# Performance work log

Measured on AMD Instinct MI355X. Metric: run time of the kernel, lower is better.

Reference implementation:

```python
import jax, jax.numpy as jnp
import numpy as np

B, N, E = 16, 5000, 160000
IN, OUT, H = 64, 64, 1  # heads=1 (GATConv default)
NEG_SLOPE = 0.2


def setup_inputs() -> dict:
    key = jax.random.key(0)
    ks = jax.random.split(key, 10)
    data = jax.random.normal(ks[0], (B, N, IN), jnp.float32)
    # random edges with no self-loops (PyG removes then re-adds self-loops;
    # with no pre-existing self-loops this matches exactly)
    src = jax.random.randint(ks[1], (E,), 0, N)
    off = jax.random.randint(ks[2], (E,), 1, N)
    dst = (src + off) % N
    edge_index = jnp.stack([src, dst]).astype(jnp.int32)
    edge_attr = jax.random.uniform(ks[3], (E,), jnp.float32)
    # GATConv parameters (glorot-ish init)
    W = jax.random.normal(ks[4], (H * OUT, IN), jnp.float32) / np.sqrt(IN)
    W_edge = jax.random.normal(ks[5], (H * OUT, 1), jnp.float32)
    att_src = jax.random.normal(ks[6], (1, H, OUT), jnp.float32) * 0.1
    att_dst = jax.random.normal(ks[7], (1, H, OUT), jnp.float32) * 0.1
    att_edge = jax.random.normal(ks[8], (1, H, OUT), jnp.float32) * 0.1
    bias = jnp.zeros((H * OUT,), jnp.float32)
    return {"data": data, "edge_index": edge_index, "edge_attr": edge_attr,
            "W": W, "W_edge": W_edge, "att_src": att_src, "att_dst": att_dst,
            "att_edge": att_edge, "bias": bias}


def reference(data, edge_index, edge_attr, W, W_edge, att_src, att_dst, att_edge, bias):
    BN = B * N
    x = data.reshape(BN, IN)
    # faithful to source: tile edges per batch WITHOUT node offset
    ei = jnp.tile(edge_index, (1, B))          # [2, B*E]
    ea = jnp.tile(edge_attr, B)[:, None]        # [B*E, 1]
    # add self-loops for all BN nodes, edge_attr filled with mean
    loops = jnp.arange(BN, dtype=ei.dtype)
    src = jnp.concatenate([ei[0], loops])       # [Etot]
    dst = jnp.concatenate([ei[1], loops])
    ea = jnp.concatenate([ea, jnp.full((BN, 1), ea.mean(), ea.dtype)])
    # linear transforms
    xl = (x @ W.T).reshape(BN, H, OUT)          # [BN, H, C]
    a_src = (xl * att_src).sum(-1)              # [BN, H]
    a_dst = (xl * att_dst).sum(-1)
    e_emb = (ea @ W_edge.T).reshape(-1, H, OUT) # [Etot, H, C]
    a_edge = (e_emb * att_edge).sum(-1)         # [Etot, H]
    # per-edge attention + segment softmax over destination nodes
    alpha = a_src[src] + a_dst[dst] + a_edge
    alpha = jax.nn.leaky_relu(alpha, NEG_SLOPE)
    amax = jax.ops.segment_max(alpha, dst, num_segments=BN)
    alpha = jnp.exp(alpha - amax[dst])
    denom = jax.ops.segment_sum(alpha, dst, num_segments=BN)
    alpha = alpha / (denom[dst] + 1e-16)
    # message passing: gather src features, weight, scatter-sum to dst
    msg = xl[src] * alpha[:, :, None]           # [Etot, H, C]
    out = jax.ops.segment_sum(msg, dst, num_segments=BN)
    out = out.reshape(BN, H * OUT) + bias
    return out.reshape(B, N, OUT), jnp.stack([src, dst]), alpha
```

## Files before the change

### kernel.cpp

```cpp
#include <hip/hip_runtime.h>

#define NN 5000
#define EE 160000
#define BNN 80000
#define BEE 2560000
#define ETOT 2640000
#define CAP 128
#define POISON ((int)0xAAAAAAAA)

#define K1_FILL 625
#define K1_GEMM 79
#define K1_SUM  80
#define K1_BLKS (K1_FILL + K1_GEMM + K1_SUM)

#define K2_GATHER 1250
#define K2_GEMMHI 1172
#define K2_OUT1   2578
#define K2_BLKS   (K2_GATHER + K2_GEMMHI + K2_OUT1)

#define K3_BLKS 1290

typedef __attribute__((ext_vector_type(8))) short short8;
typedef __attribute__((ext_vector_type(4))) float floatx4;

__device__ __forceinline__ short8 pack_bf8(const float* p) {
    union { unsigned int u[4]; short8 s; } r;
    #pragma unroll
    for (int j = 0; j < 4; ++j) {
        unsigned int lo = __float_as_uint(p[2 * j]) >> 16;
        unsigned int hi = __float_as_uint(p[2 * j + 1]) & 0xFFFF0000u;
        r.u[j] = lo | hi;
    }
    return r.s;
}

template <bool LO>
__device__ __forceinline__ void gemm_tile(
        int gblk, int t,
        const float* __restrict__ x, const float* __restrict__ W,
        const float* __restrict__ att_src, const float* __restrict__ att_dst,
        const float* __restrict__ bias,
        float* __restrict__ xl, float* __restrict__ asrc, float* __restrict__ adst,
        float* __restrict__ out0) {
    const int wave = t >> 6;
    const int lane = t & 63;
    const int quad = lane >> 4;
    const int col  = lane & 15;
    short8 bfrag[4][2];
    float attsv[4], attdv[4], biasv[4];
    #pragma unroll
    for (int ct = 0; ct < 4; ++ct) {
        int c = ct * 16 + col;
        #pragma unroll
        for (int ks = 0; ks < 2; ++ks)
            bfrag[ct][ks] = pack_bf8(W + c * 64 + ks * 32 + quad * 8);
        if (LO) { attsv[ct] = att_src[c]; attdv[ct] = att_dst[c]; }
        else    { biasv[ct] = bias[c]; }
    }
    int node0 = (gblk * 4 + wave) << 4;
    short8 afrag[2];
    const float* xrow = x + (size_t)(node0 + col) * 64;
    #pragma unroll
    for (int ks = 0; ks < 2; ++ks)
        afrag[ks] = pack_bf8(xrow + ks * 32 + quad * 8);
    floatx4 acc[4];
    #pragma unroll
    for (int ct = 0; ct < 4; ++ct) acc[ct] = (floatx4){0.f, 0.f, 0.f, 0.f};
    #pragma unroll
    for (int ks = 0; ks < 2; ++ks)
        #pragma unroll
        for (int ct = 0; ct < 4; ++ct)
            acc[ct] = __builtin_amdgcn_mfma_f32_16x16x32_bf16(afrag[ks], bfrag[ct][ks], acc[ct], 0, 0, 0);
    if (LO) {
        float ps[4] = {0.f,0.f,0.f,0.f}, pd[4] = {0.f,0.f,0.f,0.f};
        #pragma unroll
        for (int r = 0; r < 4; ++r) {
            int node = node0 + quad * 4 + r;
            #pragma unroll
            for (int ct = 0; ct < 4; ++ct) {
                float v = acc[ct][r];
                if (node < NN) xl[node * 64 + ct * 16 + col] = v;
                ps[r] += v * attsv[ct];
                pd[r] += v * attdv[ct];
            }
        }
        #pragma unroll
        for (int off = 1; off < 16; off <<= 1) {
            #pragma unroll
            for (int r = 0; r < 4; ++r) {
                ps[r] += __shfl_xor(ps[r], off, 64);
                pd[r] += __shfl_xor(pd[r], off, 64);
            }
        }
        if (col == 0) {
            #pragma unroll
            for (int r = 0; r < 4; ++r) {
                int node = node0 + quad * 4 + r;
                if (node < NN) { asrc[node] = ps[r]; adst[node] = pd[r]; }
            }
        }
    } else {
        #pragma unroll
        for (int r = 0; r < 4; ++r) {
            int node = node0 + quad * 4 + r;
            #pragma unroll
            for (int ct = 0; ct < 4; ++ct) {
                float v = acc[ct][r];
                if (node >= NN) out0[node * 64 + ct * 16 + col] = v + biasv[ct];
            }
        }
    }
}

__global__ __launch_bounds__(256) void k1(
        const float* __restrict__ x, const float* __restrict__ W,
        const float* __restrict__ att_src, const float* __restrict__ att_dst,
        const float* __restrict__ ea, const float* __restrict__ wedge,
        const float* __restrict__ atte, const int* __restrict__ ei,
        float* __restrict__ xl, float* __restrict__ asrc, float* __restrict__ adst,
        int* __restrict__ cursor, int* __restrict__ bucket, float* __restrict__ eabuf,
        float* __restrict__ partials) {
    __shared__ float red[256];
    const int blk = blockIdx.x;
    const int t = threadIdx.x;
    if (blk < K1_FILL) {
        int e = blk * 256 + t;
        int s = ei[e];
        int d = ei[EE + e];
        float ev = ea[e];
        int pos = atomicAdd(&cursor[d], 1) - POISON;
        if (pos < CAP) {
            bucket[d * CAP + pos] = (s << 18) | e;
            eabuf[d * CAP + pos] = ev;
        }
    } else if (blk < K1_FILL + K1_GEMM) {
        gemm_tile<true>(blk - K1_FILL, t, x, W, att_src, att_dst, nullptr,
                        xl, asrc, adst, nullptr);
    } else {
        int sb = blk - (K1_FILL + K1_GEMM);
        int gid = sb * 256 + t;
        float v = 0.f;
        for (int i = gid; i < EE; i += K1_SUM * 256) v += ea[i];
        red[t] = v;
        __syncthreads();
        #pragma unroll
        for (int off = 128; off > 0; off >>= 1) {
            if (t < off) red[t] += red[t + off];
            __syncthreads();
        }
        if (t == 0) partials[sb] = red[0];
        if (sb == 0 && t < 64) {
            float s = wedge[t] * atte[t];
            #pragma unroll
            for (int off = 32; off > 0; off >>= 1) s += __shfl_xor(s, off, 64);
            if (t == 0) partials[80] = s;
        }
    }
}

__global__ __launch_bounds__(256) void k2(
        const float* __restrict__ x, const float* __restrict__ W,
        const float* __restrict__ bias,
        const int* __restrict__ ei,
        const int* __restrict__ bucket, const float* __restrict__ eabuf,
        const int* __restrict__ cursor,
        const float* __restrict__ asrc, const float* __restrict__ adst,
        const float* __restrict__ partials,
        const float* __restrict__ xl,
        float* __restrict__ albuf, float* __restrict__ selfal,
        float* __restrict__ out0, float* __restrict__ out1) {
    __shared__ float s_r[4][CAP];
    __shared__ int   s_se[4][CAP];
    __shared__ int   s_e[4][CAP];
    const int blk = blockIdx.x;
    const int t = threadIdx.x, w = t >> 6, lane = t & 63;

    if (blk < K2_GATHER) {
        float s0 = 0.f;
        #pragma unroll
        for (int i = 0; i < 80; ++i) s0 += partials[i];
        float s1 = partials[80];
        float selfadd = s0 * (1.0f / EE) * s1;
        float bl = bias[lane];
        int d = blk * 4 + w;
        float* sr = s_r[w]; int* sse = s_se[w]; int* se_ = s_e[w];
        int deg = min(cursor[d] - POISON, CAP);
        float ad = adst[d];
        float rs = asrc[d] + ad + selfadd;
        rs = (rs > 0.f) ? rs : 0.2f * rs;
        float rmax = rs;
        for (int base = 0; base < deg; base += 64) {
            int idx = base + lane;
            if (idx < deg) {
                int packed = bucket[d * CAP + idx];
                float ev   = eabuf[d * CAP + idx];
                int se = packed >> 18;
                int e  = packed & 0x3FFFF;
                float r = asrc[se] + ad + ev * s1;
                r = (r > 0.f) ? r : 0.2f * r;
                sr[idx] = r; sse[idx] = se; se_[idx] = e;
                rmax = fmaxf(rmax, r);
            }
        }
        #pragma unroll
        for (int off = 32; off > 0; off >>= 1) rmax = fmaxf(rmax, __shfl_xor(rmax, off, 64));
        float m = rmax;
        float es = __expf(rs - m);
        float l = es;
        float acc = es * xl[d * 64 + lane];
        int j = 0;
        for (; j + 4 <= deg; j += 4) {
            int a0 = sse[j], a1 = sse[j + 1], a2 = sse[j + 2], a3 = sse[j + 3];
            float x0 = xl[a0 * 64 + lane], x1 = xl[a1 * 64 + lane];
            float x2 = xl[a2 * 64 + lane], x3 = xl[a3 * 64 + lane];
            float w0 = __expf(sr[j] - m),     w1 = __expf(sr[j + 1] - m);
            float w2 = __expf(sr[j + 2] - m), w3 = __expf(sr[j + 3] - m);
            acc += 16.0f * (w0 * x0 + w1 * x1 + w2 * x2 + w3 * x3);
            l   += 16.0f * (w0 + w1 + w2 + w3);
        }
        for (; j < deg; ++j) {
            float w0 = __expf(sr[j] - m);
            acc += 16.0f * w0 * xl[sse[j] * 64 + lane];
            l   += 16.0f * w0;
        }
        float inv = 1.0f / (l + 1e-16f);
        out0[d * 64 + lane] = acc * inv + bl;
        if (lane == 0) selfal[d] = es * inv;
        for (int idx = lane; idx < deg; idx += 64)
            albuf[se_[idx]] = __expf(sr[idx] - m) * inv;
    } else if (blk < K2_GATHER + K2_GEMMHI) {
        gemm_tile<false>(78 + (blk - K2_GATHER), t, x, W, nullptr, nullptr, bias,
                         nullptr, nullptr, nullptr, out0);
    } else {
        int qb = blk - (K2_GATHER + K2_GEMMHI);
        for (int q = qb * 256 + t; q < ETOT / 4; q += K2_OUT1 * 256) {
            int i = q * 4;
            float4 sv, dv;
            if (i < BEE) {
                int oe = i % EE;
                int4 s4 = *reinterpret_cast<const int4*>(ei + oe);
                int4 d4 = *reinterpret_cast<const int4*>(ei + EE + oe);
                sv = make_float4((float)s4.x, (float)s4.y, (float)s4.z, (float)s4.w);
                dv = make_float4((float)d4.x, (float)d4.y, (float)d4.z, (float)d4.w);
            } else {
                int nn = i - BEE;
                sv = make_float4((float)nn, (float)(nn+1), (float)(nn+2), (float)(nn+3));
                dv = sv;
            }
            *reinterpret_cast<float4*>(out1 + i) = sv;
            *reinterpret_cast<float4*>(out1 + ETOT + i) = dv;
        }
    }
}

__global__ __launch_bounds__(256) void k3(
        const float* __restrict__ albuf, const float* __restrict__ selfal,
        float* __restrict__ out2) {
    for (int q = blockIdx.x * 256 + threadIdx.x; q < ETOT / 4; q += K3_BLKS * 256) {
        int i = q * 4;
        float4 av;
        if (i < BEE) {
            av = *reinterpret_cast<const float4*>(albuf + (i % EE));
        } else {
            float a[4];
            #pragma unroll
            for (int jj = 0; jj < 4; ++jj) {
                int nn = i + jj - BEE;
                a[jj] = (nn < NN) ? selfal[nn] : 1.0f;
            }
            av = make_float4(a[0], a[1], a[2], a[3]);
        }
        *reinterpret_cast<float4*>(out2 + i) = av;
    }
}

extern "C" void kernel_launch(void* const* d_in, const int* in_sizes, int n_in,
                              void* d_out, int out_size, void* d_ws, size_t ws_size,
                              hipStream_t stream) {
    const float* data  = (const float*)d_in[0];
    const int*   ei    = (const int*)d_in[1];
    const float* ea    = (const float*)d_in[2];
    const float* W     = (const float*)d_in[3];
    const float* atts  = (const float*)d_in[5];
    const float* attd  = (const float*)d_in[6];
    const float* atte  = (const float*)d_in[7];
    const float* bias  = (const float*)d_in[8];
    const float* wedge = (const float*)d_in[4];

    float* out0 = (float*)d_out;
    float* out1 = out0 + 5120000;
    float* out2 = out0 + 10400000;

    float* ws = (float*)d_ws;
    float* xl       = ws;
    float* asrc     = ws + 320000;
    float* adst     = ws + 325000;
    float* albuf    = ws + 330000;
    float* selfal   = ws + 490000;
    float* partials = ws + 495000;
    int*   cursor   = (int*)(ws + 495082);
    int*   bucket   = (int*)(ws + 500082);
    float* eabuf    = ws + 1140082;

    k1<<<K1_BLKS, 256, 0, stream>>>(data, W, atts, attd, ea, wedge, atte, ei,
                                    xl, asrc, adst, cursor, bucket, eabuf, partials);
    k2<<<K2_BLKS, 256, 0, stream>>>(data, W, bias, ei, bucket, eabuf, cursor,
                                    asrc, adst, partials, xl,
                                    albuf, selfal, out0, out1);
    k3<<<K3_BLKS, 256, 0, stream>>>(albuf, selfal, out2);
}
```

Baseline: 130.1 us.

## Drop third kernel by scattering alpha directly and move high GEMM into k1

Removes the k3 launch and the albuf/selfal staging buffers. The gather kernel now writes each edge's alpha straight into all 16 batch replicas of out2, and the constant-one self-loop alphas are filled by the out1 blocks. The high-node GEMM tiles move from k2 to k1 so they overlap with bucket filling, and large output writes use nontemporal stores. In exchange, the 16-way alpha writes are scattered strided stores rather than coalesced float4 copies, which may cost write efficiency.

```diff
diff --git a/kernel.cpp b/kernel.cpp
--- a/kernel.cpp
+++ b/kernel.cpp
@@ -8,17 +8,15 @@
 #define CAP 128
 #define POISON ((int)0xAAAAAAAA)
 
-#define K1_FILL 625
-#define K1_GEMM 79
-#define K1_SUM  80
-#define K1_BLKS (K1_FILL + K1_GEMM + K1_SUM)
+#define K1_FILL   625
+#define K1_GEMMLO 79
+#define K1_SUM    80
+#define K1_GEMMHI 1172
+#define K1_BLKS (K1_FILL + K1_GEMMLO + K1_SUM + K1_GEMMHI)
 
 #define K2_GATHER 1250
-#define K2_GEMMHI 1172
 #define K2_OUT1   2578
-#define K2_BLKS   (K2_GATHER + K2_GEMMHI + K2_OUT1)
-
-#define K3_BLKS 1290
+#define K2_BLKS   (K2_GATHER + K2_OUT1)
 
 typedef __attribute__((ext_vector_type(8))) short short8;
 typedef __attribute__((ext_vector_type(4))) float floatx4;
@@ -32,6 +30,11 @@
         r.u[j] = lo | hi;
     }
     return r.s;
+}
+
+__device__ __forceinline__ void nt_store4(float a, float b, float c, float d, float* p) {
+    floatx4 v = {a, b, c, d};
+    __builtin_nontemporal_store(v, reinterpret_cast<floatx4*>(p));
 }
 
 template <bool LO>
@@ -106,7 +109,9 @@
             #pragma unroll
             for (int ct = 0; ct < 4; ++ct) {
                 float v = acc[ct][r];
-                if (node >= NN) out0[node * 64 + ct * 16 + col] = v + biasv[ct];
+                if (node >= NN)
+                    __builtin_nontemporal_store(v + biasv[ct],
+                                                &out0[node * 64 + ct * 16 + col]);
             }
         }
     }
@@ -115,9 +120,11 @@
 __global__ __launch_bounds__(256) void k1(
         const float* __restrict__ x, const float* __restrict__ W,
         const float* __restrict__ att_src, const float* __restrict__ att_dst,
+        const float* __restrict__ bias,
         const float* __restrict__ ea, const float* __restrict__ wedge,
         const float* __restrict__ atte, const int* __restrict__ ei,
         float* __restrict__ xl, float* __restrict__ asrc, float* __restrict__ adst,
+        float* __restrict__ out0,
         int* __restrict__ cursor, int* __restrict__ bucket, float* __restrict__ eabuf,
         float* __restrict__ partials) {
     __shared__ float red[256];
@@ -133,11 +140,11 @@
             bucket[d * CAP + pos] = (s << 18) | e;
             eabuf[d * CAP + pos] = ev;
         }
-    } else if (blk < K1_FILL + K1_GEMM) {
+    } else if (blk < K1_FILL + K1_GEMMLO) {
         gemm_tile<true>(blk - K1_FILL, t, x, W, att_src, att_dst, nullptr,
                         xl, asrc, adst, nullptr);
-    } else {
-        int sb = blk - (K1_FILL + K1_GEMM);
+    } else if (blk < K1_FILL + K1_GEMMLO + K1_SUM) {
+        int sb = blk - (K1_FILL + K1_GEMMLO);
         int gid = sb * 256 + t;
         float v = 0.f;
         for (int i = gid; i < EE; i += K1_SUM * 256) v += ea[i];
@@ -155,11 +162,14 @@
             for (int off = 32; off > 0; off >>= 1) s += __shfl_xor(s, off, 64);
             if (t == 0) partials[80] = s;
         }
+    } else {
+        int gblk = 78 + (blk - (K1_FILL + K1_GEMMLO + K1_SUM));
+        gemm_tile<false>(gblk, t, x, W, nullptr, nullptr, bias,
+                         nullptr, nullptr, nullptr, out0);
     }
 }
 
 __global__ __launch_bounds__(256) void k2(
-        const float* __restrict__ x, const float* __restrict__ W,
         const float* __restrict__ bias,
         const int* __restrict__ ei,
         const int* __restrict__ bucket, const float* __restrict__ eabuf,
@@ -167,8 +177,8 @@
         const float* __restrict__ asrc, const float* __restrict__ adst,
         const float* __restrict__ partials,
         const float* __restrict__ xl,
-        float* __restrict__ albuf, float* __restrict__ selfal,
-        float* __restrict__ out0, float* __restrict__ out1) {
+        float* __restrict__ out0, float* __restrict__ out1,
+        float* __restrict__ out2) {
     __shared__ float s_r[4][CAP];
     __shared__ int   s_se[4][CAP];
     __shared__ int   s_e[4][CAP];
@@ -224,53 +234,35 @@
             l   += 16.0f * w0;
         }
         float inv = 1.0f / (l + 1e-16f);
-        out0[d * 64 + lane] = acc * inv + bl;
-        if (lane == 0) selfal[d] = es * inv;
-        for (int idx = lane; idx < deg; idx += 64)
-            albuf[se_[idx]] = __expf(sr[idx] - m) * inv;
-    } else if (blk < K2_GATHER + K2_GEMMHI) {
-        gemm_tile<false>(78 + (blk - K2_GATHER), t, x, W, nullptr, nullptr, bias,
-                         nullptr, nullptr, nullptr, out0);
+        __builtin_nontemporal_store(acc * inv + bl, &out0[d * 64 + lane]);
+        if (lane == 0) out2[BEE + d] = es * inv;
+        for (int idx = lane; idx < deg; idx += 64) {
+            float a = __expf(sr[idx] - m) * inv;
+            float* p = out2 + se_[idx];
+            #pragma unroll
+            for (int b = 0; b < 16; ++b) p[b * EE] = a;
+        }
     } else {
-        int qb = blk - (K2_GATHER + K2_GEMMHI);
+        int qb = blk - K2_GATHER;
+        {
+            int idx = qb * 256 + t;
+            if (idx < (BNN - NN) / 4)
+                nt_store4(1.f, 1.f, 1.f, 1.f, out2 + BEE + NN + idx * 4);
+        }
         for (int q = qb * 256 + t; q < ETOT / 4; q += K2_OUT1 * 256) {
             int i = q * 4;
-            float4 sv, dv;
             if (i < BEE) {
                 int oe = i % EE;
                 int4 s4 = *reinterpret_cast<const int4*>(ei + oe);
                 int4 d4 = *reinterpret_cast<const int4*>(ei + EE + oe);
-                sv = make_float4((float)s4.x, (float)s4.y, (float)s4.z, (float)s4.w);
-                dv = make_float4((float)d4.x, (float)d4.y, (float)d4.z, (float)d4.w);
+                nt_store4((float)s4.x, (float)s4.y, (float)s4.z, (float)s4.w, out1 + i);
+                nt_store4((float)d4.x, (float)d4.y, (float)d4.z, (float)d4.w, out1 + ETOT + i);
             } else {
                 int nn = i - BEE;
-                sv = make_float4((float)nn, (float)(nn+1), (float)(nn+2), (float)(nn+3));
-                dv = sv;
-            }
-            *reinterpret_cast<float4*>(out1 + i) = sv;
-            *reinterpret_cast<float4*>(out1 + ETOT + i) = dv;
-        }
-    }
-}
-
-__global__ __launch_bounds__(256) void k3(
-        const float* __restrict__ albuf, const float* __restrict__ selfal,
-        float* __restrict__ out2) {
-    for (int q = blockIdx.x * 256 + threadIdx.x; q < ETOT / 4; q += K3_BLKS * 256) {
-        int i = q * 4;
-        float4 av;
-        if (i < BEE) {
-            av = *reinterpret_cast<const float4*>(albuf + (i % EE));
-        } else {
-            float a[4];
-            #pragma unroll
-            for (int jj = 0; jj < 4; ++jj) {
-                int nn = i + jj - BEE;
-                a[jj] = (nn < NN) ? selfal[nn] : 1.0f;
-            }
-            av = make_float4(a[0], a[1], a[2], a[3]);
-        }
-        *reinterpret_cast<float4*>(out2 + i) = av;
+                nt_store4((float)nn, (float)(nn+1), (float)(nn+2), (float)(nn+3), out1 + i);
+                nt_store4((float)nn, (float)(nn+1), (float)(nn+2), (float)(nn+3), out1 + ETOT + i);
+            }
+        }
     }
 }
 
@@ -281,11 +273,11 @@
     const int*   ei    = (const int*)d_in[1];
     const float* ea    = (const float*)d_in[2];
     const float* W     = (const float*)d_in[3];
+    const float* wedge = (const float*)d_in[4];
     const float* atts  = (const float*)d_in[5];
     const float* attd  = (const float*)d_in[6];
     const float* atte  = (const float*)d_in[7];
     const float* bias  = (const float*)d_in[8];
-    const float* wedge = (const float*)d_in[4];
 
     float* out0 = (float*)d_out;
     float* out1 = out0 + 5120000;
@@ -295,17 +287,15 @@
     float* xl       = ws;
     float* asrc     = ws + 320000;
     float* adst     = ws + 325000;
-    float* albuf    = ws + 330000;
-    float* selfal   = ws + 490000;
-    float* partials = ws + 495000;
-    int*   cursor   = (int*)(ws + 495082);
-    int*   bucket   = (int*)(ws + 500082);
-    float* eabuf    = ws + 1140082;
-
-    k1<<<K1_BLKS, 256, 0, stream>>>(data, W, atts, attd, ea, wedge, atte, ei,
-                                    xl, asrc, adst, cursor, bucket, eabuf, partials);
-    k2<<<K2_BLKS, 256, 0, stream>>>(data, W, bias, ei, bucket, eabuf, cursor,
+    float* partials = ws + 330000;
+    int*   cursor   = (int*)(ws + 330082);
+    int*   bucket   = (int*)(ws + 335082);
+    float* eabuf    = ws + 975082;
+
+    k1<<<K1_BLKS, 256, 0, stream>>>(data, W, atts, attd, bias, ea, wedge, atte, ei,
+                                    xl, asrc, adst, out0,
+                                    cursor, bucket, eabuf, partials);
+    k2<<<K2_BLKS, 256, 0, stream>>>(bias, ei, bucket, eabuf, cursor,
                                     asrc, adst, partials, xl,
-                                    albuf, selfal, out0, out1);
-    k3<<<K3_BLKS, 256, 0, stream>>>(albuf, selfal, out2);
-}
+                                    out0, out1, out2);
+}
```

Measured after the change: 150.3 us. 1.16x slower.
